# Performance work log

Measured on AMD Instinct MI355X. Metric: run time of the kernel, lower is better.

## Reference

```python
import jax, jax.numpy as jnp
import numpy as np

B, L, D, H, FFN = 4, 2048, 1024, 8, 2048
DH = D // H  # 128

def layer_norm(x, g, b, eps=1e-5):
    m = jnp.mean(x, axis=-1, keepdims=True)
    v = jnp.mean((x - m) ** 2, axis=-1, keepdims=True)
    return (x - m) * jax.lax.rsqrt(v + eps) * g + b

def setup_inputs() -> dict:
    key = jax.random.key(0)
    ks = jax.random.split(key, 12)
    s = 0.02
    return {
        "inputs": jax.random.normal(ks[0], (B, L, D), jnp.float32),
        "Wq": jax.random.normal(ks[1], (D, D), jnp.float32) * s,
        "bq": jnp.zeros((D,), jnp.float32),
        "Wk": jax.random.normal(ks[2], (D, D), jnp.float32) * s,
        "bk": jnp.zeros((D,), jnp.float32),
        "Wv": jax.random.normal(ks[3], (D, D), jnp.float32) * s,
        "bv": jnp.zeros((D,), jnp.float32),
        "Wo": jax.random.normal(ks[4], (D, D), jnp.float32) * s,
        "bo": jnp.zeros((D,), jnp.float32),
        "ln1_g": jnp.ones((D,), jnp.float32),
        "ln1_b": jnp.zeros((D,), jnp.float32),
        "W1": jax.random.normal(ks[5], (FFN, D), jnp.float32) * s,
        "b1": jnp.zeros((FFN,), jnp.float32),
        "W2": jax.random.normal(ks[6], (D, FFN), jnp.float32) * s,
        "b2": jnp.zeros((D,), jnp.float32),
        "ln2_g": jnp.ones((D,), jnp.float32),
        "ln2_b": jnp.zeros((D,), jnp.float32),
    }

def reference(inputs, Wq, bq, Wk, bk, Wv, bv, Wo, bo, ln1_g, ln1_b, W1, b1, W2, b2, ln2_g, ln2_b):
    b, l, d = inputs.shape
    # linear projections then the original's raw row-major view (no head transpose)
    q = (inputs @ Wq.T + bq).reshape(b * H, -1, DH)
    k = (inputs @ Wk.T + bk).reshape(b * H, -1, DH)
    v = (inputs @ Wv.T + bv).reshape(b * H, -1, DH)
    scale = DH ** -0.5  # (2 * (d_k//2))^-0.5 in the original
    atten = jax.nn.softmax(jnp.einsum('bqd,bkd->bqk', q, k) * scale, axis=-1)
    context = jnp.einsum('bqk,bkd->bqd', atten, v).reshape(b, -1, H * DH)
    out = context @ Wo.T + bo
    h = layer_norm(inputs + out, ln1_g, ln1_b)  # residual + LN (dropout=0)
    # PositionwiseFeedForward: 1x1 conv1d == per-token linear
    f = jax.nn.relu(h @ W1.T + b1) @ W2.T + b2
    y = layer_norm(h + f, ln2_g, ln2_b)
    return (y, atten)
```

## Files before the change

kernel.cpp:

```cpp
#include <hip/hip_runtime.h>
#include <stdint.h>

using f32x4  = __attribute__((ext_vector_type(4))) float;
using f32x16 = __attribute__((ext_vector_type(16))) float;
using bf16x8 = __attribute__((ext_vector_type(8))) short;

#define DEV static __device__ __forceinline__

DEV unsigned short f2bf(float f){
  union { float f; unsigned int u; } c; c.f = f;
  unsigned int u = c.u;
  u += 0x7FFFu + ((u >> 16) & 1u);
  return (unsigned short)(u >> 16);
}
DEV float bf2f(unsigned short u){
  union { unsigned int u; float f; } c; c.u = ((unsigned int)u) << 16; return c.f;
}

DEV void gld_lds16(const void* g, void* l){
  __builtin_amdgcn_global_load_lds(
      (const __attribute__((address_space(1))) void*)g,
      (__attribute__((address_space(3))) void*)l, 16, 0, 0);
}

__global__ __launch_bounds__(256) void cvt_f32_bf16(
    const float* __restrict__ in, unsigned short* __restrict__ out, int n){
  for (int i = (blockIdx.x*256 + threadIdx.x)*4; i < n; i += gridDim.x*1024){
    float4 v = *(const float4*)(in + i);
    ushort4 o; o.x=f2bf(v.x); o.y=f2bf(v.y); o.z=f2bf(v.z); o.w=f2bf(v.w);
    *(ushort4*)(out + i) = o;
  }
}

template<bool OUT_BF16, bool RELU, bool HAS_BIAS>
__global__ __launch_bounds__(256, 2)
void gemm_bt(const unsigned short* __restrict__ Ap, const unsigned short* __restrict__ Bp,
             const float* __restrict__ bias, void* __restrict__ Cp, int N, int K)
{
  constexpr int BM = 128, BN = 128, BK = 32;
  __shared__ __align__(16) unsigned short As[BM*BK];
  __shared__ __align__(16) unsigned short Bs[BN*BK];
  const int tid  = threadIdx.x;
  const int lane = tid & 63;
  const int wid  = tid >> 6;
  const int wr   = wid >> 1, wc = wid & 1;
  const int mrow = lane & 15;
  const int krow = lane >> 4;

  const unsigned short* Ab = Ap + (long)blockIdx.y*BM*K;
  const unsigned short* Bb = Bp + (long)blockIdx.x*BN*K;

  f32x4 acc[4][4] = {};

  for (int k0 = 0; k0 < K; k0 += BK){
    #pragma unroll
    for (int it = 0; it < 2; ++it){
      int ci  = it*256 + tid;
      int row = ci >> 2;
      int col = (ci & 3) * 8;
      gld_lds16(Ab + (long)row*K + k0 + col, (char*)As + it*4096 + wid*1024);
    }
    #pragma unroll
    for (int it = 0; it < 2; ++it){
      int ci  = it*256 + tid;
      int row = ci >> 2;
      int col = (ci & 3) * 8;
      gld_lds16(Bb + (long)row*K + k0 + col, (char*)Bs + it*4096 + wid*1024);
    }
    __syncthreads();

    bf16x8 a[4], b[4];
    #pragma unroll
    for (int mi = 0; mi < 4; ++mi)
      a[mi] = *(const bf16x8*)&As[(wr*64 + mi*16 + mrow)*BK + krow*8];
    #pragma unroll
    for (int ni = 0; ni < 4; ++ni)
      b[ni] = *(const bf16x8*)&Bs[(wc*64 + ni*16 + mrow)*BK + krow*8];
    #pragma unroll
    for (int mi = 0; mi < 4; ++mi)
      #pragma unroll
      for (int ni = 0; ni < 4; ++ni)
        acc[mi][ni] = __builtin_amdgcn_mfma_f32_16x16x32_bf16(a[mi], b[ni], acc[mi][ni], 0, 0, 0);
    __syncthreads();
  }

  int row0 = blockIdx.y*BM + wr*64;
  int col0 = blockIdx.x*BN + wc*64;
  #pragma unroll
  for (int mi = 0; mi < 4; ++mi){
    #pragma unroll
    for (int ni = 0; ni < 4; ++ni){
      int col = col0 + ni*16 + mrow;
      float bv = HAS_BIAS ? bias[col] : 0.f;
      #pragma unroll
      for (int r = 0; r < 4; ++r){
        int row = row0 + mi*16 + krow*4 + r;
        float v = acc[mi][ni][r] + bv;
        if (RELU) v = fmaxf(v, 0.f);
        if (OUT_BF16) ((unsigned short*)Cp)[(long)row*N + col] = f2bf(v);
        else          ((float*)Cp)[(long)row*N + col] = v;
      }
    }
  }
}

__global__ __launch_bounds__(256) void transpose_v(
    const unsigned short* __restrict__ V, unsigned short* __restrict__ Vt){
  __shared__ unsigned short t[32][33];
  int g = blockIdx.z;
  int j0 = blockIdx.x*32, e0 = blockIdx.y*32;
  int tx = threadIdx.x, ty = threadIdx.y;
  const unsigned short* Vg = V + (long)g*262144;
  unsigned short* Vtg = Vt + (long)g*262144;
  #pragma unroll
  for (int i = 0; i < 4; ++i)
    t[ty + 8*i][tx] = Vg[(long)(j0 + ty + 8*i)*128 + e0 + tx];
  __syncthreads();
  #pragma unroll
  for (int i = 0; i < 4; ++i)
    Vtg[(long)(e0 + ty + 8*i)*2048 + j0 + tx] = t[tx][ty + 8*i];
}

__global__ __launch_bounds__(256, 2) void attn_fused(
    const unsigned short* __restrict__ Q, const unsigned short* __restrict__ K,
    const unsigned short* __restrict__ Vt, float* __restrict__ P,
    unsigned short* __restrict__ CTX)
{
  __shared__ __align__(16) char lds[65536];
  char* ldsK = lds;
  char* ldsV = lds + 32768;
  const int tid  = threadIdx.x;
  const int lane = tid & 63;
  const int w    = tid >> 6;
  const int l31  = lane & 31;
  const int hi   = lane >> 5;
  const float scale = 0.08838834764831845f;

  const int d  = blockIdx.x;
  const int i  = d >> 3;
  const int g  = (d & 7) + 8*(i >> 4);
  const int q0 = (i & 15) * 128;

  const char* KbB = (const char*)(K  + (size_t)g*262144);
  const char* VtB = (const char*)(Vt + (size_t)g*262144);
  const unsigned short* Qb = Q + (size_t)g*262144 + (size_t)(q0 + w*32)*128;
  float* Pb = P + (size_t)g*4194304 + (size_t)(q0 + w*32)*2048;

  bf16x8 qf[8];
  #pragma unroll
  for (int kk = 0; kk < 8; ++kk)
    qf[kk] = *(const bf16x8*)((const char*)Qb + (size_t)l31*256 + kk*32 + hi*16);

  auto stageK = [&](int buf, int j0b){
    #pragma unroll
    for (int r = 0; r < 4; ++r){
      int o = r*4096 + tid*16;
      int j = o >> 8, c = o & 255;
      gld_lds16(KbB + (size_t)(j0b + j)*256 + (c ^ ((j & 15) << 4)),
                ldsK + buf*16384 + o);
    }
  };
  auto stageV = [&](int buf, int j0b){
    #pragma unroll
    for (int r = 0; r < 4; ++r){
      int o = r*4096 + tid*16;
      int e = o >> 7, c = o & 127;
      gld_lds16(VtB + (size_t)e*4096 + j0b*2 + (c ^ ((e & 7) << 4)),
                ldsV + buf*16384 + o);
    }
  };
  auto readK = [&](int buf, int jloc, int kk) -> bf16x8 {
    int row = jloc + l31;
    int col = (kk*32 + hi*16) ^ ((l31 & 15) << 4);
    return *(const bf16x8*)(ldsK + buf*16384 + row*256 + col);
  };
  auto readV = [&](int buf, int jloc, int c16, int t) -> bf16x8 {
    int row = t*32 + l31;
    int col = (jloc*2 + c16*32 + hi*16) ^ ((row & 7) << 4);
    return *(const bf16x8*)(ldsV + buf*16384 + row*128 + col);
  };

  int buf = 0;
  stageK(0, 0);
  __syncthreads();
  float lacc = 0.f;
  for (int st = 0; st < 32; ++st){
    if (st < 31) stageK(buf ^ 1, (st + 1) * 64);
    #pragma unroll
    for (int jt = 0; jt < 2; ++jt){
      const int jloc = jt * 32;
      f32x16 s1 = {}, s2 = {};
      #pragma unroll
      for (int kk = 0; kk < 4; ++kk){
        s1 = __builtin_amdgcn_mfma_f32_32x32x16_bf16(readK(buf, jloc, kk),   qf[kk],   s1, 0, 0, 0);
        s2 = __builtin_amdgcn_mfma_f32_32x32x16_bf16(readK(buf, jloc, kk+4), qf[kk+4], s2, 0, 0, 0);
      }
      #pragma unroll
      for (int r = 0; r < 16; ++r) lacc += __expf((s1[r] + s2[r]) * scale);
    }
    __syncthreads();
    buf ^= 1;
  }
  lacc += __shfl_xor(lacc, 32, 64);
  const float invl = 1.f / lacc;

  stageK(0, 0); stageV(0, 0);
  __syncthreads();
  f32x16 O[4] = {};
  buf = 0;
  for (int st = 0; st < 32; ++st){
    if (st < 31){ stageK(buf ^ 1, (st + 1) * 64); stageV(buf ^ 1, (st + 1) * 64); }
    #pragma unroll
    for (int jt = 0; jt < 2; ++jt){
      const int jloc  = jt * 32;
      const int jglob = st*64 + jloc;
      f32x16 s1 = {}, s2 = {};
      #pragma unroll
      for (int kk = 0; kk < 4; ++kk){
        s1 = __builtin_amdgcn_mfma_f32_32x32x16_bf16(readK(buf, jloc, kk),   qf[kk],   s1, 0, 0, 0);
        s2 = __builtin_amdgcn_mfma_f32_32x32x16_bf16(readK(buf, jloc, kk+4), qf[kk+4], s2, 0, 0, 0);
      }
      float p[16];
      #pragma unroll
      for (int r = 0; r < 16; ++r) p[r] = __expf((s1[r] + s2[r]) * scale) * invl;
      float* prow = Pb + (size_t)l31*2048 + jglob + hi*4;
      *(float4*)(prow)      = make_float4(p[0],  p[1],  p[2],  p[3]);
      *(float4*)(prow + 8)  = make_float4(p[4],  p[5],  p[6],  p[7]);
      *(float4*)(prow + 16) = make_float4(p[8],  p[9],  p[10], p[11]);
      *(float4*)(prow + 24) = make_float4(p[12], p[13], p[14], p[15]);
      unsigned int pk[8];
      #pragma unroll
      for (int ii = 0; ii < 8; ++ii)
        pk[ii] = (unsigned int)f2bf(p[2*ii]) | ((unsigned int)f2bf(p[2*ii+1]) << 16);
      unsigned int r0 = (unsigned int)__shfl_xor((int)(hi ? pk[0] : pk[2]), 32, 64);
      unsigned int r1 = (unsigned int)__shfl_xor((int)(hi ? pk[1] : pk[3]), 32, 64);
      unsigned int r2 = (unsigned int)__shfl_xor((int)(hi ? pk[4] : pk[6]), 32, 64);
      unsigned int r3 = (unsigned int)__shfl_xor((int)(hi ? pk[5] : pk[7]), 32, 64);
      union U { unsigned int u[4]; bf16x8 v; };
      U a0, a1;
      a0.u[0] = hi ? r0    : pk[0];  a0.u[1] = hi ? r1    : pk[1];
      a0.u[2] = hi ? pk[2] : r0;     a0.u[3] = hi ? pk[3] : r1;
      a1.u[0] = hi ? r2    : pk[4];  a1.u[1] = hi ? r3    : pk[5];
      a1.u[2] = hi ? pk[6] : r2;     a1.u[3] = hi ? pk[7] : r3;
      #pragma unroll
      for (int t = 0; t < 4; ++t){
        O[t] = __builtin_amdgcn_mfma_f32_32x32x16_bf16(a0.v, readV(buf, jloc, 0, t), O[t], 0, 0, 0);
        O[t] = __builtin_amdgcn_mfma_f32_32x32x16_bf16(a1.v, readV(buf, jloc, 1, t), O[t], 0, 0, 0);
      }
    }
    __syncthreads();
    buf ^= 1;
  }

  #pragma unroll
  for (int t = 0; t < 4; ++t){
    #pragma unroll
    for (int r = 0; r < 16; ++r){
      int qrow = (r & 3) + 8*(r >> 2) + 4*hi;
      CTX[(size_t)g*262144 + (size_t)(q0 + w*32 + qrow)*128 + t*32 + l31] = f2bf(O[t][r]);
    }
  }
}

DEV float block_sum256(float v, float* red){
  #pragma unroll
  for (int off = 32; off > 0; off >>= 1) v += __shfl_xor(v, off, 64);
  int lane = threadIdx.x & 63, wid = threadIdx.x >> 6;
  if (lane == 0) red[wid] = v;
  __syncthreads();
  return (red[0]+red[1]) + (red[2]+red[3]);
}

template<bool WRITE_F32, bool WRITE_BF>
__global__ __launch_bounds__(256) void ln_residual_bf(
    const unsigned short* __restrict__ A, const unsigned short* __restrict__ R,
    const float* __restrict__ gamma, const float* __restrict__ beta,
    float* __restrict__ outf, unsigned short* __restrict__ outb){
  __shared__ float red1[4], red2[4];
  long base = (long)blockIdx.x * 1024;
  int tid = threadIdx.x;
  ushort4 a = *(const ushort4*)(A + base + tid*4);
  ushort4 r = *(const ushort4*)(R + base + tid*4);
  float v[4] = { bf2f(a.x)+bf2f(r.x), bf2f(a.y)+bf2f(r.y),
                 bf2f(a.z)+bf2f(r.z), bf2f(a.w)+bf2f(r.w) };
  float s = (v[0]+v[1]) + (v[2]+v[3]);
  s = block_sum256(s, red1);
  float mean = s * (1.f/1024.f);
  float dd[4] = {v[0]-mean, v[1]-mean, v[2]-mean, v[3]-mean};
  float sq = (dd[0]*dd[0]+dd[1]*dd[1]) + (dd[2]*dd[2]+dd[3]*dd[3]);
  sq = block_sum256(sq, red2);
  float rstd = rsqrtf(sq*(1.f/1024.f) + 1e-5f);
  float4 g4 = *(const float4*)(gamma + tid*4);
  float4 b4 = *(const float4*)(beta  + tid*4);
  float o[4] = { dd[0]*rstd*g4.x + b4.x, dd[1]*rstd*g4.y + b4.y,
                 dd[2]*rstd*g4.z + b4.z, dd[3]*rstd*g4.w + b4.w };
  if (WRITE_F32){
    float4 o4; o4.x=o[0]; o4.y=o[1]; o4.z=o[2]; o4.w=o[3];
    *(float4*)(outf + base + tid*4) = o4;
  }
  if (WRITE_BF){
    ushort4 ob; ob.x=f2bf(o[0]); ob.y=f2bf(o[1]); ob.z=f2bf(o[2]); ob.w=f2bf(o[3]);
    *(ushort4*)(outb + base + tid*4) = ob;
  }
}

extern "C" void kernel_launch(void* const* d_in, const int* in_sizes, int n_in,
                              void* d_out, int out_size, void* d_ws, size_t ws_size,
                              hipStream_t stream){
  const float* X   = (const float*)d_in[0];
  const float* Wq  = (const float*)d_in[1];
  const float* bq  = (const float*)d_in[2];
  const float* Wk  = (const float*)d_in[3];
  const float* bk  = (const float*)d_in[4];
  const float* Wv  = (const float*)d_in[5];
  const float* bv  = (const float*)d_in[6];
  const float* Wo  = (const float*)d_in[7];
  const float* bo  = (const float*)d_in[8];
  const float* g1  = (const float*)d_in[9];
  const float* b1n = (const float*)d_in[10];
  const float* W1  = (const float*)d_in[11];
  const float* b1  = (const float*)d_in[12];
  const float* W2  = (const float*)d_in[13];
  const float* b2  = (const float*)d_in[14];
  const float* g2  = (const float*)d_in[15];
  const float* b2n = (const float*)d_in[16];

  const int M = 8192, D = 1024, F = 2048;
  const long YSZ = (long)M * D;
  float* y_out = (float*)d_out;
  float* atten = (float*)d_out + YSZ;

  char* w = (char*)d_ws;
  auto alloc = [&](size_t bytes){ char* p = w; w += (bytes + 255) & ~(size_t)255; return p; };
  unsigned short* Xbf   = (unsigned short*)alloc((size_t)M*D*2);
  unsigned short* Wqbf  = (unsigned short*)alloc((size_t)D*D*2);
  unsigned short* Wkbf  = (unsigned short*)alloc((size_t)D*D*2);
  unsigned short* Wvbf  = (unsigned short*)alloc((size_t)D*D*2);
  unsigned short* Wobf  = (unsigned short*)alloc((size_t)D*D*2);
  unsigned short* W1bf  = (unsigned short*)alloc((size_t)F*D*2);
  unsigned short* W2bf  = (unsigned short*)alloc((size_t)D*F*2);
  unsigned short* Qbf   = (unsigned short*)alloc((size_t)M*D*2);
  unsigned short* Kbf   = (unsigned short*)alloc((size_t)M*D*2);
  unsigned short* Vbf   = (unsigned short*)alloc((size_t)M*D*2);
  unsigned short* Vtbf  = (unsigned short*)alloc((size_t)M*D*2);
  unsigned short* CTXbf = (unsigned short*)alloc((size_t)M*D*2);
  unsigned short* Hbf   = (unsigned short*)alloc((size_t)M*D*2);
  unsigned short* F1bf  = (unsigned short*)alloc((size_t)M*F*2);
  unsigned short* TMPbf = (unsigned short*)alloc((size_t)M*D*2);

  auto cvt = [&](const float* src, unsigned short* dst, int n){
    int blocks = (n/4 + 255)/256; if (blocks > 4096) blocks = 4096;
    cvt_f32_bf16<<<blocks, 256, 0, stream>>>(src, dst, n);
  };
  cvt(X,  Xbf,  M*D);
  cvt(Wq, Wqbf, D*D);  cvt(Wk, Wkbf, D*D);  cvt(Wv, Wvbf, D*D);  cvt(Wo, Wobf, D*D);
  cvt(W1, W1bf, F*D);  cvt(W2, W2bf, D*F);

  dim3 blk(256);

  gemm_bt<true,false,true><<<dim3(D/128, M/128), blk, 0, stream>>>(Xbf, Wqbf, bq, Qbf, D, D);
  gemm_bt<true,false,true><<<dim3(D/128, M/128), blk, 0, stream>>>(Xbf, Wkbf, bk, Kbf, D, D);
  gemm_bt<true,false,true><<<dim3(D/128, M/128), blk, 0, stream>>>(Xbf, Wvbf, bv, Vbf, D, D);

  transpose_v<<<dim3(64, 4, 32), dim3(32, 8), 0, stream>>>(Vbf, Vtbf);

  attn_fused<<<dim3(512), dim3(256), 0, stream>>>(Qbf, Kbf, Vtbf, atten, CTXbf);

  gemm_bt<true,false,true><<<dim3(D/128, M/128), blk, 0, stream>>>(CTXbf, Wobf, bo, TMPbf, D, D);

  ln_residual_bf<false,true><<<M, 256, 0, stream>>>(Xbf, TMPbf, g1, b1n, nullptr, Hbf);

  gemm_bt<true,true,true><<<dim3(F/128, M/128), blk, 0, stream>>>(Hbf, W1bf, b1, F1bf, F, D);

  gemm_bt<true,false,true><<<dim3(D/128, M/128), blk, 0, stream>>>(F1bf, W2bf, b2, TMPbf, D, F);

  ln_residual_bf<true,false><<<M, 256, 0, stream>>>(Hbf, TMPbf, g2, b2n, y_out, nullptr);
}
```

Baseline: 509.7 us.

## Replace GEMM with 256x128 tile, multi-stage LDS pipeline, swizzle and XCD remap

```diff
diff --git a/kernel.cpp b/kernel.cpp
--- a/kernel.cpp
+++ b/kernel.cpp
@@ -33,63 +33,105 @@
 }
 
 template<bool OUT_BF16, bool RELU, bool HAS_BIAS>
-__global__ __launch_bounds__(256, 2)
-void gemm_bt(const unsigned short* __restrict__ Ap, const unsigned short* __restrict__ Bp,
-             const float* __restrict__ bias, void* __restrict__ Cp, int N, int K)
+__global__ __launch_bounds__(512, 2)
+void gemm_bt2(const unsigned short* __restrict__ Ap, const unsigned short* __restrict__ Bp,
+              const float* __restrict__ bias, void* __restrict__ Cp, int N, int K)
 {
-  constexpr int BM = 128, BN = 128, BK = 32;
-  __shared__ __align__(16) unsigned short As[BM*BK];
-  __shared__ __align__(16) unsigned short Bs[BN*BK];
+  __shared__ __align__(16) char lds[131072];
   const int tid  = threadIdx.x;
   const int lane = tid & 63;
   const int wid  = tid >> 6;
-  const int wr   = wid >> 1, wc = wid & 1;
+  const int wm   = wid >> 2;
+  const int wn   = wid & 3;
   const int mrow = lane & 15;
   const int krow = lane >> 4;
 
-  const unsigned short* Ab = Ap + (long)blockIdx.y*BM*K;
-  const unsigned short* Bb = Bp + (long)blockIdx.x*BN*K;
-
-  f32x4 acc[4][4] = {};
-
-  for (int k0 = 0; k0 < K; k0 += BK){
-    #pragma unroll
-    for (int it = 0; it < 2; ++it){
-      int ci  = it*256 + tid;
-      int row = ci >> 2;
-      int col = (ci & 3) * 8;
-      gld_lds16(Ab + (long)row*K + k0 + col, (char*)As + it*4096 + wid*1024);
-    }
-    #pragma unroll
-    for (int it = 0; it < 2; ++it){
-      int ci  = it*256 + tid;
-      int row = ci >> 2;
-      int col = (ci & 3) * 8;
-      gld_lds16(Bb + (long)row*K + k0 + col, (char*)Bs + it*4096 + wid*1024);
-    }
-    __syncthreads();
-
-    bf16x8 a[4], b[4];
-    #pragma unroll
-    for (int mi = 0; mi < 4; ++mi)
-      a[mi] = *(const bf16x8*)&As[(wr*64 + mi*16 + mrow)*BK + krow*8];
-    #pragma unroll
-    for (int ni = 0; ni < 4; ++ni)
-      b[ni] = *(const bf16x8*)&Bs[(wc*64 + ni*16 + mrow)*BK + krow*8];
-    #pragma unroll
-    for (int mi = 0; mi < 4; ++mi)
-      #pragma unroll
-      for (int ni = 0; ni < 4; ++ni)
-        acc[mi][ni] = __builtin_amdgcn_mfma_f32_16x16x32_bf16(a[mi], b[ni], acc[mi][ni], 0, 0, 0);
-    __syncthreads();
-  }
-
-  int row0 = blockIdx.y*BM + wr*64;
-  int col0 = blockIdx.x*BN + wc*64;
-  #pragma unroll
-  for (int mi = 0; mi < 4; ++mi){
-    #pragma unroll
-    for (int ni = 0; ni < 4; ++ni){
+  const int nbx = N >> 7;
+  const int nwg = gridDim.x;
+  const int d   = blockIdx.x;
+  const int swz = (d & 7)*(nwg >> 3) + (d >> 3);
+  const int bx  = swz % nbx, by = swz / nbx;
+
+  const size_t Kb = (size_t)K * 2;
+  const char* Ab = (const char*)(Ap + (size_t)by*256*K);
+  const char* Bb = (const char*)(Bp + (size_t)bx*128*K);
+  const int NT = K >> 6;
+
+  auto stageA = [&](int t){
+    char* dst = lds + (t % 3)*32768;
+    const char* src = Ab + (size_t)t*128;
+    #pragma unroll
+    for (int s = 0; s < 4; ++s){
+      int o = s*8192 + tid*16;
+      int row = o >> 7, cb = o & 127;
+      gld_lds16(src + (size_t)row*Kb + (cb ^ ((row & 7) << 4)), dst + o);
+    }
+  };
+  auto stageB = [&](int t){
+    char* dst = lds + 98304 + (t & 1)*16384;
+    const char* src = Bb + (size_t)t*128;
+    #pragma unroll
+    for (int s = 0; s < 2; ++s){
+      int o = s*8192 + tid*16;
+      int row = o >> 7, cb = o & 127;
+      gld_lds16(src + (size_t)row*Kb + (cb ^ ((row & 7) << 4)), dst + o);
+    }
+  };
+
+  f32x4 acc[8][2] = {};
+
+  stageA(0); stageB(0); stageA(1);
+  asm volatile("s_waitcnt vmcnt(4)" ::: "memory");
+  __builtin_amdgcn_s_barrier();
+
+  for (int t = 0; t < NT; ++t){
+    if (t + 1 < NT) stageB(t + 1);
+    if (t + 2 < NT) stageA(t + 2);
+
+    const char* baseA = lds + (t % 3)*32768;
+    const char* baseB = lds + 98304 + (t & 1)*16384;
+
+    bf16x8 b[2][2];
+    #pragma unroll
+    for (int ni = 0; ni < 2; ++ni){
+      int row = wn*32 + ni*16 + mrow;
+      #pragma unroll
+      for (int ks = 0; ks < 2; ++ks)
+        b[ni][ks] = *(const bf16x8*)(baseB + row*128 + ((ks*64 + krow*16) ^ ((row & 7) << 4)));
+    }
+    bf16x8 a[8][2];
+    #pragma unroll
+    for (int mi = 0; mi < 8; ++mi){
+      int row = wm*128 + mi*16 + mrow;
+      #pragma unroll
+      for (int ks = 0; ks < 2; ++ks)
+        a[mi][ks] = *(const bf16x8*)(baseA + row*128 + ((ks*64 + krow*16) ^ ((row & 7) << 4)));
+    }
+
+    __builtin_amdgcn_s_setprio(1);
+    #pragma unroll
+    for (int ks = 0; ks < 2; ++ks)
+      #pragma unroll
+      for (int mi = 0; mi < 8; ++mi)
+        #pragma unroll
+        for (int ni = 0; ni < 2; ++ni)
+          acc[mi][ni] = __builtin_amdgcn_mfma_f32_16x16x32_bf16(a[mi][ks], b[ni][ks], acc[mi][ni], 0, 0, 0);
+    __builtin_amdgcn_s_setprio(0);
+
+    if (t + 1 < NT){
+      if (t + 2 < NT) asm volatile("s_waitcnt vmcnt(4)" ::: "memory");
+      else            asm volatile("s_waitcnt vmcnt(0)" ::: "memory");
+      __builtin_amdgcn_s_barrier();
+      __builtin_amdgcn_sched_barrier(0);
+    }
+  }
+
+  int row0 = by*256 + wm*128;
+  int col0 = bx*128 + wn*32;
+  #pragma unroll
+  for (int mi = 0; mi < 8; ++mi){
+    #pragma unroll
+    for (int ni = 0; ni < 2; ++ni){
       int col = col0 + ni*16 + mrow;
       float bv = HAS_BIAS ? bias[col] : 0.f;
       #pragma unroll
@@ -97,8 +139,8 @@
         int row = row0 + mi*16 + krow*4 + r;
         float v = acc[mi][ni][r] + bv;
         if (RELU) v = fmaxf(v, 0.f);
-        if (OUT_BF16) ((unsigned short*)Cp)[(long)row*N + col] = f2bf(v);
-        else          ((float*)Cp)[(long)row*N + col] = v;
+        if (OUT_BF16) ((unsigned short*)Cp)[(size_t)row*N + col] = f2bf(v);
+        else          ((float*)Cp)[(size_t)row*N + col] = v;
       }
     }
   }
@@ -356,23 +398,23 @@
   cvt(Wq, Wqbf, D*D);  cvt(Wk, Wkbf, D*D);  cvt(Wv, Wvbf, D*D);  cvt(Wo, Wobf, D*D);
   cvt(W1, W1bf, F*D);  cvt(W2, W2bf, D*F);
 
-  dim3 blk(256);
-
-  gemm_bt<true,false,true><<<dim3(D/128, M/128), blk, 0, stream>>>(Xbf, Wqbf, bq, Qbf, D, D);
-  gemm_bt<true,false,true><<<dim3(D/128, M/128), blk, 0, stream>>>(Xbf, Wkbf, bk, Kbf, D, D);
-  gemm_bt<true,false,true><<<dim3(D/128, M/128), blk, 0, stream>>>(Xbf, Wvbf, bv, Vbf, D, D);
+  dim3 blk2(512);
+
+  gemm_bt2<true,false,true><<<dim3((M/256)*(D/128)), blk2, 0, stream>>>(Xbf, Wqbf, bq, Qbf, D, D);
+  gemm_bt2<true,false,true><<<dim3((M/256)*(D/128)), blk2, 0, stream>>>(Xbf, Wkbf, bk, Kbf, D, D);
+  gemm_bt2<true,false,true><<<dim3((M/256)*(D/128)), blk2, 0, stream>>>(Xbf, Wvbf, bv, Vbf, D, D);
 
   transpose_v<<<dim3(64, 4, 32), dim3(32, 8), 0, stream>>>(Vbf, Vtbf);
 
   attn_fused<<<dim3(512), dim3(256), 0, stream>>>(Qbf, Kbf, Vtbf, atten, CTXbf);
 
-  gemm_bt<true,false,true><<<dim3(D/128, M/128), blk, 0, stream>>>(CTXbf, Wobf, bo, TMPbf, D, D);
+  gemm_bt2<true,false,true><<<dim3((M/256)*(D/128)), blk2, 0, stream>>>(CTXbf, Wobf, bo, TMPbf, D, D);
 
   ln_residual_bf<false,true><<<M, 256, 0, stream>>>(Xbf, TMPbf, g1, b1n, nullptr, Hbf);
 
-  gemm_bt<true,true,true><<<dim3(F/128, M/128), blk, 0, stream>>>(Hbf, W1bf, b1, F1bf, F, D);
-
-  gemm_bt<true,false,true><<<dim3(D/128, M/128), blk, 0, stream>>>(F1bf, W2bf, b2, TMPbf, D, F);
+  gemm_bt2<true,true,true><<<dim3((M/256)*(F/128)), blk2, 0, stream>>>(Hbf, W1bf, b1, F1bf, F, D);
+
+  gemm_bt2<true,false,true><<<dim3((M/256)*(D/128)), blk2, 0, stream>>>(F1bf, W2bf, b2, TMPbf, D, F);
 
   ln_residual_bf<true,false><<<M, 256, 0, stream>>>(Hbf, TMPbf, g2, b2n, y_out, nullptr);
 }
```

New measurement: 459.4 us. -9.9%, faster.
